# Performance work log

Hardware: AMD Instinct MI355X
Metric: run time of the kernel (lower is better)

The kernel has to match this reference:

```python
import jax, jax.numpy as jnp
import numpy as np

HIDDEN = 2048
HEADS = 16
HEAD_DIM = HIDDEN // HEADS  # 128
B, S = 2, 2048


def setup_inputs() -> dict:
    key = jax.random.key(0)
    ks = jax.random.split(key, 9)
    s_in = 1.0 / np.sqrt(HIDDEN)
    return {
        "X": jax.random.normal(ks[0], (B, S, HIDDEN), dtype=jnp.float32),
        "attention_mask": jnp.ones((B, S, S), dtype=jnp.int32),
        "Wq": jax.random.uniform(ks[1], (HIDDEN, HIDDEN), jnp.float32, -s_in, s_in),
        "bq": jax.random.uniform(ks[2], (HIDDEN,), jnp.float32, -s_in, s_in),
        "Wk": jax.random.uniform(ks[3], (HIDDEN, HEAD_DIM), jnp.float32, -s_in, s_in),
        "bk": jax.random.uniform(ks[4], (HEAD_DIM,), jnp.float32, -s_in, s_in),
        "Wv": jax.random.uniform(ks[5], (HIDDEN, HEAD_DIM), jnp.float32, -s_in, s_in),
        "bv": jax.random.uniform(ks[6], (HEAD_DIM,), jnp.float32, -s_in, s_in),
        "Wo": jax.random.uniform(ks[7], (HIDDEN, HIDDEN), jnp.float32, -s_in, s_in),
        "bo": jax.random.uniform(ks[8], (HIDDEN,), jnp.float32, -s_in, s_in),
    }


def reference(X, attention_mask, Wq, bq, Wk, bk, Wv, bv, Wo, bo):
    b, s, _ = X.shape
    # Projections
    Q = X @ Wq + bq                      # (B, S, H*D)
    K = X @ Wk + bk                      # (B, S, D)  shared across heads (MQA)
    V = X @ Wv + bv                      # (B, S, D)
    Q = Q.reshape(b, s, HEADS, HEAD_DIM).transpose(0, 2, 1, 3)  # (B, H, S, D)
    scale = 1.0 / jnp.sqrt(jnp.float32(HEAD_DIM))
    # QK^T with shared K head
    scores = jnp.einsum('bhqd,bkd->bhqk', Q, K) * scale          # (B, H, S, S)
    scores = jnp.where(attention_mask[:, None, :, :] == 0, -jnp.inf, scores)
    attn = jax.nn.softmax(scores, axis=-1)
    # dropout_rate = 0.0 (eval) -> identity
    out = jnp.einsum('bhqk,bkd->bhqd', attn, V)                  # (B, H, S, D)
    out = out.transpose(0, 2, 1, 3).reshape(b, s, HIDDEN)        # (B, S, hidden)
    return out @ Wo + bo
```

## Files before the change

### kernel.cpp

```cpp
#include <hip/hip_runtime.h>
#include <cstdint>
#include <cstddef>

#define HIDDEN 2048
#define HEADS 16
#define HD 128
#define BSZ 2
#define SEQ 2048
#define MTOT (BSZ * SEQ)
#define NQKV (HIDDEN + 2 * HD)
#define SL2E 0.12751743f

typedef unsigned short ushort_t;
typedef __attribute__((ext_vector_type(8))) __bf16 bf16x8;
typedef __attribute__((ext_vector_type(4))) float f32x4;
typedef __attribute__((ext_vector_type(16))) float f32x16;

typedef __attribute__((address_space(3))) unsigned int as3_u32;
typedef __attribute__((address_space(1))) const unsigned int as1_u32;

__device__ __forceinline__ ushort_t f2bf(float x) {
  union { float f; unsigned u; } v; v.f = x;
  unsigned r = v.u + 0x7fffu + ((v.u >> 16) & 1u);
  return (ushort_t)(r >> 16);
}
__device__ __forceinline__ unsigned pk_bf16(float a, float b) {
  union { float f; unsigned u; } x, y; x.f = a; y.f = b;
  return (x.u >> 16) | (y.u & 0xFFFF0000u);
}

__device__ __forceinline__ void gld16(const void* g, void* lds) {
  __builtin_amdgcn_global_load_lds((as1_u32*)g, (as3_u32*)lds, 16, 0, 0);
}

#define PREP_NM (32 * 16 * BSZ)
#define PREP_N0 (MTOT * HIDDEN / 4 / 256)
#define PREP_N1 ((NQKV / 32) * (HIDDEN / 32))
#define PREP_N2 ((HIDDEN / 32) * (HIDDEN / 32))
#define PREP_N4 ((NQKV + 255) / 256)
#define PREP_NB (PREP_NM + PREP_N0 + PREP_N1 + PREP_N2 + PREP_N4)

__global__ __launch_bounds__(256) void prep_kernel(
    const float* __restrict__ X, ushort_t* __restrict__ Xb,
    const float* __restrict__ Wq, const float* __restrict__ Wk,
    const float* __restrict__ Wv, ushort_t* __restrict__ WT,
    const float* __restrict__ Wo, ushort_t* __restrict__ WoT,
    const int* __restrict__ mask, int* __restrict__ flags,
    const float* __restrict__ bq, const float* __restrict__ bk,
    const float* __restrict__ bv, float* __restrict__ biasQKV) {
  __shared__ float tileF[32][36];
  __shared__ int sAO[8];
  const int t = threadIdx.x;
  int j = blockIdx.x;

  if (j < PREP_NM) {
    const int kt = j & 31, qt = (j >> 5) & 15, b = j >> 9;
    int allv = 1, anyv = 0;
    const size_t base = (size_t)b * SEQ * SEQ + (size_t)qt * 128 * SEQ + kt * 64;
    for (int i = t; i < 2048; i += 256) {
      const int row = i >> 4, c4 = (i & 15) << 2;
      const int4 v = *(const int4*)(mask + base + (size_t)row * SEQ + c4);
      const int nz = (v.x != 0) & (v.y != 0) & (v.z != 0) & (v.w != 0);
      const int nzany = (v.x != 0) | (v.y != 0) | (v.z != 0) | (v.w != 0);
      allv &= nz; anyv |= nzany;
    }
    const int wAll = __all(allv), wAny = __any(anyv);
    if ((t & 63) == 0) { sAO[t >> 6] = wAll; sAO[4 + (t >> 6)] = wAny; }
    __syncthreads();
    if (t == 0) {
      const int A = sAO[0] & sAO[1] & sAO[2] & sAO[3];
      const int O = sAO[4] | sAO[5] | sAO[6] | sAO[7];
      flags[(b * 16 + qt) * 32 + kt] = A ? 2 : (O ? 1 : 0);
    }
    return;
  }
  j -= PREP_NM;

  if (j < PREP_N0) {
    const int i = j * 256 + t;
    float4 v = ((const float4*)X)[i];
    ushort4 o;
    o.x = f2bf(v.x); o.y = f2bf(v.y); o.z = f2bf(v.z); o.w = f2bf(v.w);
    ((ushort4*)Xb)[i] = o;
    return;
  }
  j -= PREP_N0;

  if (j < PREP_N1) {
    const int nb = (j % (NQKV / 32)) * 32, kb = (j / (NQKV / 32)) * 32;
    const float* W; int N, nc; float scale;
    if (nb < HIDDEN)           { W = Wq; N = HIDDEN; nc = nb;               scale = SL2E; }
    else if (nb < HIDDEN + HD) { W = Wk; N = HD;     nc = nb - HIDDEN;      scale = 1.f; }
    else                       { W = Wv; N = HD;     nc = nb - HIDDEN - HD; scale = 1.f; }
    {
      int row = t >> 3, c4 = (t & 7) << 2;
      float4 v = *(const float4*)(W + (size_t)(kb + row) * N + nc + c4);
      tileF[row][c4] = v.x * scale; tileF[row][c4 + 1] = v.y * scale;
      tileF[row][c4 + 2] = v.z * scale; tileF[row][c4 + 3] = v.w * scale;
    }
    __syncthreads();
    {
      int nl = t >> 3, k4 = (t & 7) << 2;
      ushort4 o;
      o.x = f2bf(tileF[k4 + 0][nl]); o.y = f2bf(tileF[k4 + 1][nl]);
      o.z = f2bf(tileF[k4 + 2][nl]); o.w = f2bf(tileF[k4 + 3][nl]);
      *(ushort4*)(WT + (size_t)(nb + nl) * HIDDEN + kb + k4) = o;
    }
    return;
  }
  j -= PREP_N1;

  if (j < PREP_N2) {
    const int nb = (j % (HIDDEN / 32)) * 32, kb = (j / (HIDDEN / 32)) * 32;
    {
      int row = t >> 3, c4 = (t & 7) << 2;
      float4 v = *(const float4*)(Wo + (size_t)(kb + row) * HIDDEN + nb + c4);
      tileF[row][c4] = v.x; tileF[row][c4 + 1] = v.y;
      tileF[row][c4 + 2] = v.z; tileF[row][c4 + 3] = v.w;
    }
    __syncthreads();
    {
      int nl = t >> 3, k4 = (t & 7) << 2;
      ushort4 o;
      o.x = f2bf(tileF[k4 + 0][nl]); o.y = f2bf(tileF[k4 + 1][nl]);
      o.z = f2bf(tileF[k4 + 2][nl]); o.w = f2bf(tileF[k4 + 3][nl]);
      *(ushort4*)(WoT + (size_t)(nb + nl) * HIDDEN + kb + k4) = o;
    }
    return;
  }
  j -= PREP_N2;

  {
    const int i = j * 256 + t;
    if (i < NQKV)
      biasQKV[i] = (i < HIDDEN) ? bq[i] * SL2E
                 : (i < HIDDEN + HD ? bk[i - HIDDEN] : bv[i - HIDDEN - HD]);
  }
}

template <int OUTF32, int FUSEV>
__global__ __launch_bounds__(256) void gemm_mfma(
    const ushort_t* __restrict__ A, const ushort_t* __restrict__ Bt,
    const float* __restrict__ bias, void* __restrict__ C,
    ushort_t* __restrict__ Vt, int M, int N, int K, int nm_per_xcd) {
  __shared__ ushort_t Smem[4 * 128 * 64];
  ushort_t (*As)[128 * 64] = reinterpret_cast<ushort_t(*)[128 * 64]>(Smem);
  ushort_t (*Bs)[128 * 64] =
      reinterpret_cast<ushort_t(*)[128 * 64]>(Smem + 2 * 128 * 64);
  const int t = threadIdx.x;
  const int w = t >> 6, l = t & 63;
  const int id = blockIdx.x;
  const int xcd = id & 7, j = id >> 3;
  const int mt = xcd * nm_per_xcd + (j % nm_per_xcd);
  const int nt = j / nm_per_xcd;
  const int mb = mt * 128, nb = nt * 128;
  const int wm = (w >> 1) * 64, wn = (w & 1) * 64;
  const int fl = l & 15, g = l >> 4;
  const int srow = l >> 3, cphys = l & 7;

  f32x4 acc[4][4];
#pragma unroll
  for (int i = 0; i < 4; ++i)
#pragma unroll
    for (int jj = 0; jj < 4; ++jj) acc[i][jj] = (f32x4){0.f, 0.f, 0.f, 0.f};

#pragma unroll
  for (int jj = 0; jj < 4; ++jj) {
    const int inst = w * 4 + jj;
    const int row = inst * 8 + srow;
    const int clog = cphys ^ (row & 7);
    gld16(A + (size_t)(mb + row) * K + clog * 8, &As[0][inst * 512]);
    gld16(Bt + (size_t)(nb + row) * K + clog * 8, &Bs[0][inst * 512]);
  }

  int cur = 0;
  for (int k0 = 0; k0 < K; k0 += 64) {
    __syncthreads();
    if (k0 + 64 < K) {
#pragma unroll
      for (int jj = 0; jj < 4; ++jj) {
        const int inst = w * 4 + jj;
        const int row = inst * 8 + srow;
        const int clog = cphys ^ (row & 7);
        gld16(A + (size_t)(mb + row) * K + k0 + 64 + clog * 8,
              &As[cur ^ 1][inst * 512]);
        gld16(Bt + (size_t)(nb + row) * K + k0 + 64 + clog * 8,
              &Bs[cur ^ 1][inst * 512]);
      }
    }
    const ushort_t* Ac = &As[cur][0];
    const ushort_t* Bc = &Bs[cur][0];
#pragma unroll
    for (int s = 0; s < 2; ++s) {
      bf16x8 af[4], bfr[4];
#pragma unroll
      for (int i = 0; i < 4; ++i) {
        const int m = wm + i * 16 + fl;
        af[i] = *(const bf16x8*)&Ac[m * 64 + (((s << 2) + g) ^ (m & 7)) * 8];
        const int n = wn + i * 16 + fl;
        bfr[i] = *(const bf16x8*)&Bc[n * 64 + (((s << 2) + g) ^ (n & 7)) * 8];
      }
#pragma unroll
      for (int i = 0; i < 4; ++i)
#pragma unroll
        for (int jj = 0; jj < 4; ++jj)
          acc[i][jj] = __builtin_amdgcn_mfma_f32_16x16x32_bf16(
              af[i], bfr[jj], acc[i][jj], 0, 0, 0);
    }
    cur ^= 1;
  }

  const bool dofv = FUSEV && (nb == HIDDEN + HD);
  if (dofv) __syncthreads();

#pragma unroll
  for (int jj = 0; jj < 4; ++jj) {
    const int col = nb + wn + jj * 16 + fl;
    const float bv = bias[col];
#pragma unroll
    for (int i = 0; i < 4; ++i) {
      const int row0 = mb + wm + i * 16 + g * 4;
#pragma unroll
      for (int r = 0; r < 4; ++r) {
        const float val = acc[i][jj][r] + bv;
        if (OUTF32) {
          ((float*)C)[(size_t)(row0 + r) * N + col] = val;
        } else {
          const ushort_t bb = f2bf(val);
          ((ushort_t*)C)[(size_t)(row0 + r) * N + col] = bb;
          if (dofv) {
            const int cl = wn + jj * 16 + fl;
            const int rl = row0 - mb + r;
            Smem[cl * 132 + rl] = bb;
          }
        }
      }
    }
  }

  if (dofv) {
    __syncthreads();
    const int c4 = (t & 31) * 4;
#pragma unroll
    for (int k = 0; k < 16; ++k) {
      const int d = k * 8 + (t >> 5);
      const ushort4 v = *(const ushort4*)&Smem[d * 132 + c4];
      *(ushort4*)(Vt + (size_t)d * MTOT + mb + c4) = v;
    }
  }
}

__global__ __launch_bounds__(256, 2) void flash_mfma(
    const ushort_t* __restrict__ QKV,
    const ushort_t* __restrict__ Vt,
    const int* __restrict__ mask,
    const int* __restrict__ flags,
    ushort_t* __restrict__ Ab)
{
  __shared__ ushort_t Kbuf[2][64 * 128];
  __shared__ ushort_t Vbuf[64 * 128];

  const int qt = blockIdx.x, h = blockIdx.y, b = blockIdx.z;
  const int t = threadIdx.x, w = t >> 6, l = t & 63;
  const int q31 = l & 31, hi = l >> 5;
  const int qbase = qt * 128;
  const int qrow = qbase + w * 32 + q31;

  bf16x8 qf[8];
#pragma unroll
  for (int ks = 0; ks < 8; ++ks)
    qf[ks] = *(const bf16x8*)(QKV + (size_t)(b * SEQ + qrow) * NQKV + h * HD +
                              ks * 16 + hi * 8);

  bf16x8 onesf;
  {
    const ushort_t ov = (q31 == 0) ? (ushort_t)0x3F80 : (ushort_t)0;
#pragma unroll
    for (int jj = 0; jj < 8; ++jj) ((ushort_t*)&onesf)[jj] = ov;
  }

#pragma unroll
  for (int j = 0; j < 4; ++j) {
    const int inst = w * 4 + j;
    const int krow = inst * 4 + (l >> 4);
    const int ck = (l & 15) ^ (krow & 15);
    gld16(QKV + (size_t)(b * SEQ + krow) * NQKV + HIDDEN + ck * 8,
          &Kbuf[0][inst * 512]);
  }

  const size_t mbase = (size_t)b * SEQ * SEQ;

  f32x16 oacc[4], lacc;
#pragma unroll
  for (int d = 0; d < 4; ++d)
#pragma unroll
    for (int r = 0; r < 16; ++r) oacc[d][r] = 0.f;
#pragma unroll
  for (int r = 0; r < 16; ++r) lacc[r] = 0.f;

  int cur = 0;
  for (int kt = 0; kt < SEQ / 64; ++kt) {
    const int kbase = kt * 64;
    const int flag = flags[((b * 16 + qt) << 5) + kt];
    __syncthreads();

#pragma unroll
    for (int j = 0; j < 4; ++j) {
      const int inst = w * 4 + j;
      const int vr = inst * 4 + (l >> 4);
      const int clog = (l & 15) ^ (vr & 15);
      const int d = 2 * vr + (clog >> 3);
      gld16(Vt + (size_t)d * MTOT + b * SEQ + kbase + (clog & 7) * 8,
            &Vbuf[inst * 512]);
    }
    {
      const int knb = (kt + 1 < SEQ / 64) ? (kbase + 64) : kbase;
#pragma unroll
      for (int j = 0; j < 4; ++j) {
        const int inst = w * 4 + j;
        const int krow = inst * 4 + (l >> 4);
        const int ck = (l & 15) ^ (krow & 15);
        gld16(QKV + (size_t)(b * SEQ + knb + krow) * NQKV + HIDDEN + ck * 8,
              &Kbuf[cur ^ 1][inst * 512]);
      }
    }

    const ushort_t* Kc = &Kbuf[cur][0];
    f32x16 sc[2];
#pragma unroll
    for (int kk = 0; kk < 2; ++kk)
#pragma unroll
      for (int r = 0; r < 16; ++r) sc[kk][r] = 0.f;

    __builtin_amdgcn_s_setprio(1);
#pragma unroll
    for (int ks = 0; ks < 8; ++ks)
#pragma unroll
      for (int kk = 0; kk < 2; ++kk) {
        const int key = kk * 32 + q31;
        const bf16x8 kf = *(const bf16x8*)&Kc[key * 128 +
                                              (((ks << 1) + hi) ^ (key & 15)) * 8];
        sc[kk] = __builtin_amdgcn_mfma_f32_32x32x16_bf16(kf, qf[ks], sc[kk],
                                                         0, 0, 0);
      }
    __builtin_amdgcn_s_setprio(0);

    if (flag != 2) {
#pragma unroll
      for (int kk = 0; kk < 2; ++kk)
#pragma unroll
        for (int r = 0; r < 16; ++r) {
          const int key = kbase + kk * 32 + (r & 3) + ((r >> 2) << 3) + (hi << 2);
          if (!mask[mbase + (size_t)qrow * SEQ + key]) sc[kk][r] = -1e30f;
        }
    }

    bf16x8 pa[4];
#pragma unroll
    for (int kk = 0; kk < 2; ++kk) {
      float pv[16];
#pragma unroll
      for (int r = 0; r < 16; ++r) pv[r] = __builtin_amdgcn_exp2f(sc[kk][r]);
#pragma unroll
      for (int half = 0; half < 2; ++half) {
        const int bs = half * 8;
        unsigned a0 = pk_bf16(pv[bs + 0], pv[bs + 1]);
        unsigned a1 = pk_bf16(pv[bs + 2], pv[bs + 3]);
        unsigned b0 = pk_bf16(pv[bs + 4], pv[bs + 5]);
        unsigned b1 = pk_bf16(pv[bs + 6], pv[bs + 7]);
        asm("v_permlane32_swap_b32 %0, %1" : "+v"(a0), "+v"(b0));
        asm("v_permlane32_swap_b32 %0, %1" : "+v"(a1), "+v"(b1));
        union { unsigned u[4]; bf16x8 v; } uu;
        uu.u[0] = a0; uu.u[1] = a1; uu.u[2] = b0; uu.u[3] = b1;
        pa[kk * 2 + half] = uu.v;
      }
    }

    asm volatile("s_waitcnt vmcnt(4)" ::: "memory");
    __builtin_amdgcn_s_barrier();
    asm volatile("" ::: "memory");
    __builtin_amdgcn_sched_barrier(0);

    __builtin_amdgcn_s_setprio(1);
#pragma unroll
    for (int ks = 0; ks < 4; ++ks) {
#pragma unroll
      for (int dt = 0; dt < 4; ++dt) {
        const int d = dt * 32 + q31;
        const int vr = d >> 1;
        const int clog = ((d & 1) << 3) + (ks << 1) + hi;
        const bf16x8 vf =
            *(const bf16x8*)&Vbuf[vr * 128 + (clog ^ (vr & 15)) * 8];
        oacc[dt] = __builtin_amdgcn_mfma_f32_32x32x16_bf16(pa[ks], vf,
                                                           oacc[dt], 0, 0, 0);
      }
      lacc = __builtin_amdgcn_mfma_f32_32x32x16_bf16(pa[ks], onesf, lacc,
                                                     0, 0, 0);
    }
    __builtin_amdgcn_s_setprio(0);
    cur ^= 1;
  }

#pragma unroll
  for (int r = 0; r < 16; ++r) {
    const float ls = __shfl(lacc[r], l & 32, 64);
    const float invl = 1.0f / ls;
    const int row = b * SEQ + qbase + w * 32 + (r & 3) + ((r >> 2) << 3) +
                    (hi << 2);
#pragma unroll
    for (int dt = 0; dt < 4; ++dt)
      Ab[(size_t)row * HIDDEN + h * HD + dt * 32 + q31] =
          f2bf(oacc[dt][r] * invl);
  }
}

extern "C" void kernel_launch(void* const* d_in, const int* in_sizes, int n_in,
                              void* d_out, int out_size, void* d_ws, size_t ws_size,
                              hipStream_t stream) {
  const float* X  = (const float*)d_in[0];
  const int* mask = (const int*)d_in[1];
  const float* Wq = (const float*)d_in[2];
  const float* bq = (const float*)d_in[3];
  const float* Wk = (const float*)d_in[4];
  const float* bk = (const float*)d_in[5];
  const float* Wv = (const float*)d_in[6];
  const float* bv = (const float*)d_in[7];
  const float* Wo = (const float*)d_in[8];
  const float* bo = (const float*)d_in[9];
  float* out = (float*)d_out;

  char* p = (char*)d_ws;
  int* flags     = (int*)p;      p += BSZ * 16 * 32 * 4;
  float* biasQKV = (float*)p;    p += 16384;
  ushort_t* QKVb = (ushort_t*)p; p += (size_t)MTOT * NQKV * 2;
  ushort_t* Xb   = (ushort_t*)p; p += (size_t)MTOT * HIDDEN * 2;
  ushort_t* WT   = (ushort_t*)p; p += (size_t)NQKV * HIDDEN * 2;
  ushort_t* WoT  = (ushort_t*)p; p += (size_t)HIDDEN * HIDDEN * 2;
  ushort_t* Vt   = (ushort_t*)p; p += (size_t)HD * MTOT * 2;
  ushort_t* Ab = Xb;

  prep_kernel<<<PREP_NB, 256, 0, stream>>>(
      X, Xb, Wq, Wk, Wv, WT, Wo, WoT, mask, flags, bq, bk, bv, biasQKV);

  gemm_mfma<0, 1><<<dim3((MTOT / 128) * (NQKV / 128)), 256, 0, stream>>>(
      Xb, WT, biasQKV, QKVb, Vt, MTOT, NQKV, HIDDEN, (MTOT / 128) / 8);
  flash_mfma<<<dim3(SEQ / 128, HEADS, BSZ), 256, 0, stream>>>(
      QKVb, Vt, mask, flags, Ab);
  gemm_mfma<1, 0><<<dim3((MTOT / 128) * (HIDDEN / 128)), 256, 0, stream>>>(
      Ab, WoT, bo, out, nullptr, MTOT, HIDDEN, HIDDEN, (MTOT / 128) / 8);
}
```

Before: 312.7 us.

## Shrink GEMM tiles to 128x64 and replace double buffering with single-buffered LDS

```diff
diff --git a/kernel.cpp b/kernel.cpp
--- a/kernel.cpp
+++ b/kernel.cpp
@@ -143,78 +143,74 @@
     const ushort_t* __restrict__ A, const ushort_t* __restrict__ Bt,
     const float* __restrict__ bias, void* __restrict__ C,
     ushort_t* __restrict__ Vt, int M, int N, int K, int nm_per_xcd) {
-  __shared__ ushort_t Smem[4 * 128 * 64];
-  ushort_t (*As)[128 * 64] = reinterpret_cast<ushort_t(*)[128 * 64]>(Smem);
-  ushort_t (*Bs)[128 * 64] =
-      reinterpret_cast<ushort_t(*)[128 * 64]>(Smem + 2 * 128 * 64);
+  __shared__ ushort_t As[128 * 64];
+  __shared__ ushort_t Bs[64 * 64];
   const int t = threadIdx.x;
   const int w = t >> 6, l = t & 63;
   const int id = blockIdx.x;
   const int xcd = id & 7, j = id >> 3;
   const int mt = xcd * nm_per_xcd + (j % nm_per_xcd);
   const int nt = j / nm_per_xcd;
-  const int mb = mt * 128, nb = nt * 128;
-  const int wm = (w >> 1) * 64, wn = (w & 1) * 64;
+  const int mb = mt * 128, nb = nt * 64;
+  const int wm = (w >> 1) * 64, wn = (w & 1) * 32;
   const int fl = l & 15, g = l >> 4;
   const int srow = l >> 3, cphys = l & 7;
 
-  f32x4 acc[4][4];
+  auto stage = [&](int kt) {
+#pragma unroll
+    for (int jj = 0; jj < 4; ++jj) {
+      const int inst = w * 4 + jj;
+      const int row = inst * 8 + srow;
+      const int cl = cphys ^ (row & 7);
+      gld16(A + (size_t)(mb + row) * K + kt * 64 + cl * 8, &As[inst * 512]);
+    }
+#pragma unroll
+    for (int jj = 0; jj < 2; ++jj) {
+      const int inst = w * 2 + jj;
+      const int row = inst * 8 + srow;
+      const int cl = cphys ^ (row & 7);
+      gld16(Bt + (size_t)(nb + row) * K + kt * 64 + cl * 8, &Bs[inst * 512]);
+    }
+  };
+
+  f32x4 acc[4][2];
 #pragma unroll
   for (int i = 0; i < 4; ++i)
 #pragma unroll
-    for (int jj = 0; jj < 4; ++jj) acc[i][jj] = (f32x4){0.f, 0.f, 0.f, 0.f};
-
-#pragma unroll
-  for (int jj = 0; jj < 4; ++jj) {
-    const int inst = w * 4 + jj;
-    const int row = inst * 8 + srow;
-    const int clog = cphys ^ (row & 7);
-    gld16(A + (size_t)(mb + row) * K + clog * 8, &As[0][inst * 512]);
-    gld16(Bt + (size_t)(nb + row) * K + clog * 8, &Bs[0][inst * 512]);
-  }
-
-  int cur = 0;
-  for (int k0 = 0; k0 < K; k0 += 64) {
-    __syncthreads();
-    if (k0 + 64 < K) {
-#pragma unroll
-      for (int jj = 0; jj < 4; ++jj) {
-        const int inst = w * 4 + jj;
-        const int row = inst * 8 + srow;
-        const int clog = cphys ^ (row & 7);
-        gld16(A + (size_t)(mb + row) * K + k0 + 64 + clog * 8,
-              &As[cur ^ 1][inst * 512]);
-        gld16(Bt + (size_t)(nb + row) * K + k0 + 64 + clog * 8,
-              &Bs[cur ^ 1][inst * 512]);
-      }
-    }
-    const ushort_t* Ac = &As[cur][0];
-    const ushort_t* Bc = &Bs[cur][0];
+    for (int jj = 0; jj < 2; ++jj) acc[i][jj] = (f32x4){0.f, 0.f, 0.f, 0.f};
+
+  stage(0);
+  __syncthreads();
+  const int nsteps = K >> 6;
+  for (int it = 0; it < nsteps; ++it) {
 #pragma unroll
     for (int s = 0; s < 2; ++s) {
-      bf16x8 af[4], bfr[4];
+      bf16x8 af[4], bfr[2];
 #pragma unroll
       for (int i = 0; i < 4; ++i) {
         const int m = wm + i * 16 + fl;
-        af[i] = *(const bf16x8*)&Ac[m * 64 + (((s << 2) + g) ^ (m & 7)) * 8];
-        const int n = wn + i * 16 + fl;
-        bfr[i] = *(const bf16x8*)&Bc[n * 64 + (((s << 2) + g) ^ (n & 7)) * 8];
+        af[i] = *(const bf16x8*)&As[m * 64 + (((s << 2) + g) ^ (m & 7)) * 8];
+      }
+#pragma unroll
+      for (int jj = 0; jj < 2; ++jj) {
+        const int n = wn + jj * 16 + fl;
+        bfr[jj] = *(const bf16x8*)&Bs[n * 64 + (((s << 2) + g) ^ (n & 7)) * 8];
       }
 #pragma unroll
       for (int i = 0; i < 4; ++i)
 #pragma unroll
-        for (int jj = 0; jj < 4; ++jj)
+        for (int jj = 0; jj < 2; ++jj)
           acc[i][jj] = __builtin_amdgcn_mfma_f32_16x16x32_bf16(
               af[i], bfr[jj], acc[i][jj], 0, 0, 0);
     }
-    cur ^= 1;
-  }
-
-  const bool dofv = FUSEV && (nb == HIDDEN + HD);
-  if (dofv) __syncthreads();
-
-#pragma unroll
-  for (int jj = 0; jj < 4; ++jj) {
+    __syncthreads();
+    if (it + 1 < nsteps) stage(it + 1);
+    __syncthreads();
+  }
+
+  const bool dofv = FUSEV && (nb >= HIDDEN + HD);
+#pragma unroll
+  for (int jj = 0; jj < 2; ++jj) {
     const int col = nb + wn + jj * 16 + fl;
     const float bv = bias[col];
 #pragma unroll
@@ -231,7 +227,7 @@
           if (dofv) {
             const int cl = wn + jj * 16 + fl;
             const int rl = row0 - mb + r;
-            Smem[cl * 132 + rl] = bb;
+            As[cl * 128 + (rl ^ ((cl & 15) << 3))] = bb;
           }
         }
       }
@@ -240,12 +236,14 @@
 
   if (dofv) {
     __syncthreads();
-    const int c4 = (t & 31) * 4;
-#pragma unroll
-    for (int k = 0; k < 16; ++k) {
-      const int d = k * 8 + (t >> 5);
-      const ushort4 v = *(const ushort4*)&Smem[d * 132 + c4];
-      *(ushort4*)(Vt + (size_t)d * MTOT + mb + c4) = v;
+    const int vbase = nb - (HIDDEN + HD);
+    const int rl4 = (t & 31) * 4;
+#pragma unroll
+    for (int k = 0; k < 8; ++k) {
+      const int dl = k * 8 + (t >> 5);
+      const ushort4 v =
+          *(const ushort4*)&As[dl * 128 + (rl4 ^ ((dl & 15) << 3))];
+      *(ushort4*)(Vt + (size_t)(vbase + dl) * MTOT + mb + rl4) = v;
     }
   }
 }
@@ -442,10 +440,10 @@
   prep_kernel<<<PREP_NB, 256, 0, stream>>>(
       X, Xb, Wq, Wk, Wv, WT, Wo, WoT, mask, flags, bq, bk, bv, biasQKV);
 
-  gemm_mfma<0, 1><<<dim3((MTOT / 128) * (NQKV / 128)), 256, 0, stream>>>(
+  gemm_mfma<0, 1><<<dim3((MTOT / 128) * (NQKV / 64)), 256, 0, stream>>>(
       Xb, WT, biasQKV, QKVb, Vt, MTOT, NQKV, HIDDEN, (MTOT / 128) / 8);
   flash_mfma<<<dim3(SEQ / 128, HEADS, BSZ), 256, 0, stream>>>(
       QKVb, Vt, mask, flags, Ab);
-  gemm_mfma<1, 0><<<dim3((MTOT / 128) * (HIDDEN / 128)), 256, 0, stream>>>(
+  gemm_mfma<1, 0><<<dim3((MTOT / 128) * (HIDDEN / 64)), 256, 0, stream>>>(
       Ab, WoT, bo, out, nullptr, MTOT, HIDDEN, HIDDEN, (MTOT / 128) / 8);
 }
```

Result: slower. 331.3 us (+6.0%).
